# Optimization experiments

Measured on AMD Instinct MI355X. Metric: run time of the kernel, lower is better.

Reference implementation:

```python
import jax, jax.numpy as jnp
import numpy as np

E = 8        # n_experts
K = 2        # top_k
D = 1024     # n_embed
H = 2048     # moe_n_hidden
B, T = 4, 2048


def setup_inputs() -> dict:
    key = jax.random.key(0)
    ks = jax.random.split(key, 6)
    s = 0.02
    return {
        "x": jax.random.normal(ks[0], (B, T, D), dtype=jnp.float32),
        "Wr": jax.random.normal(ks[1], (D, E), dtype=jnp.float32) * s,   # router weight
        "W1": jax.random.normal(ks[2], (E, D, 2 * H), dtype=jnp.float32) * s,
        "b1": jnp.zeros((E, 2 * H), dtype=jnp.float32),
        "W2": jax.random.normal(ks[3], (E, H, D), dtype=jnp.float32) * s,
        "b2": jnp.zeros((E, D), dtype=jnp.float32),
    }


def reference(x, Wr, W1, b1, W2, b2):
    b, t, d = x.shape
    # router logits (noise=0, temp=1.0)
    z = jnp.einsum('btd,de->bte', x, Wr)                 # [B,T,E]
    vals, idx = jax.lax.top_k(z, K)                      # [B,T,K]
    gates = jax.nn.softmax(vals, axis=-1)                # [B,T,K]
    # combine weights per (token, expert): sum_k gate_k * 1[idx_k == e]
    onehot = jax.nn.one_hot(idx, E, dtype=x.dtype)       # [B,T,K,E]
    comb = jnp.einsum('btk,btke->bte', gates, onehot).reshape(b * t, E)
    xf = x.reshape(b * t, d)                             # [N,D]
    out = jnp.zeros_like(xf)
    for e in range(E):  # fixed small loop over structurally-distinct experts
        ab = xf @ W1[e] + b1[e]                          # [N,2H]
        a, bb = jnp.split(ab, 2, axis=-1)
        h = jax.nn.silu(a) * bb                          # swiGLU
        y = h @ W2[e] + b2[e]                            # [N,D]
        out = out + comb[:, e:e + 1] * y
    return out.reshape(b, t, d)
```

## Files before the change

### kernel.cpp

```cpp
#include <hip/hip_runtime.h>


#define N_TOK 8192
#define DIM   1024
#define HID   2048
#define NEXP  8
#define NK    (N_TOK * 2)
#define MAXT1 136
#define G1Y   272

typedef __attribute__((ext_vector_type(8))) short short8;
typedef __attribute__((ext_vector_type(4))) float f32x4;

#define BARX() __builtin_amdgcn_s_barrier()
#define FEN()  asm volatile("" ::: "memory")
#define VMW4() asm volatile("s_waitcnt vmcnt(4)" ::: "memory")
#define VMW0() asm volatile("s_waitcnt vmcnt(0)" ::: "memory")
#define PRIO(p) __builtin_amdgcn_s_setprio(p)

static __device__ __forceinline__ unsigned short f2bf(float f) {
  unsigned int u = __float_as_uint(f);
  u += 0x7fffu + ((u >> 16) & 1u);
  return (unsigned short)(u >> 16);
}

static __device__ __forceinline__ void glds16(const void* g, void* l) {
  __builtin_amdgcn_global_load_lds(
      (const __attribute__((address_space(1))) unsigned int*)g,
      (__attribute__((address_space(3))) unsigned int*)l, 16, 0, 0);
}

__device__ __forceinline__ void transpose_tile(const float* __restrict__ s,
                                               unsigned short* __restrict__ d,
                                               int R, int C, int c0, int r0,
                                               unsigned short (*tT)[68]) {
  int tid = threadIdx.x;
  int c = tid & 63, rq = tid >> 6;
#pragma unroll
  for (int q = 0; q < 4; ++q) {
    int rb = q * 16 + rq * 4;
    ushort4 v;
    v.x = f2bf(s[(size_t)(r0 + rb + 0) * C + c0 + c]);
    v.y = f2bf(s[(size_t)(r0 + rb + 1) * C + c0 + c]);
    v.z = f2bf(s[(size_t)(r0 + rb + 2) * C + c0 + c]);
    v.w = f2bf(s[(size_t)(r0 + rb + 3) * C + c0 + c]);
    *(ushort4*)&tT[c][rb] = v;
  }
  __syncthreads();
#pragma unroll
  for (int it = 0; it < 4; ++it) {
    int idx = it * 256 + tid;
    int cc = idx >> 4;
    int r4 = (idx & 15) * 4;
    *(ushort4*)(d + (size_t)(c0 + cc) * R + r0 + r4) = *(const ushort4*)&tT[cc][r4];
  }
}

__global__ __launch_bounds__(256) void prep_k(
    const float* __restrict__ x, const float* __restrict__ Wr,
    const float* __restrict__ W1,
    unsigned short* __restrict__ w1t,
    unsigned short* __restrict__ xb, int* __restrict__ te,
    float* __restrict__ tg) {
  __shared__ unsigned short tT[64][68];
  int bid = blockIdx.x;
  if (bid < 8192) {
    int z = bid >> 10, rem = bid & 1023;
    int c0 = (rem & 63) * 64, r0 = (rem >> 6) * 64;
    transpose_tile(W1 + (size_t)z * DIM * 2 * HID,
                   w1t + (size_t)z * DIM * 2 * HID, DIM, 2 * HID, c0, r0, tT);
  } else {
    int n = (bid - 8192) * 4 + (threadIdx.x >> 6);
    int lane = threadIdx.x & 63;
    float z[8];
#pragma unroll
    for (int e = 0; e < 8; ++e) z[e] = 0.f;
    const float* xr = x + (size_t)n * DIM;
    unsigned short* xbr = xb + (size_t)n * DIM;
#pragma unroll 4
    for (int i = 0; i < DIM / 64; ++i) {
      int d = lane + i * 64;
      float xv = xr[d];
      xbr[d] = f2bf(xv);
      float4 w0 = *(const float4*)(Wr + (size_t)d * 8);
      float4 w1 = *(const float4*)(Wr + (size_t)d * 8 + 4);
      z[0] += xv * w0.x; z[1] += xv * w0.y; z[2] += xv * w0.z; z[3] += xv * w0.w;
      z[4] += xv * w1.x; z[5] += xv * w1.y; z[6] += xv * w1.z; z[7] += xv * w1.w;
    }
    for (int off = 32; off; off >>= 1)
#pragma unroll
      for (int e = 0; e < 8; ++e) z[e] += __shfl_down(z[e], off);
    if (lane == 0) {
      int e0 = 0; float v0 = z[0];
#pragma unroll
      for (int e = 1; e < 8; ++e) if (z[e] > v0) { v0 = z[e]; e0 = e; }
      int e1 = -1; float v1 = -3.4e38f;
#pragma unroll
      for (int e = 0; e < 8; ++e) if (e != e0 && z[e] > v1) { v1 = z[e]; e1 = e; }
      float r = expf(v1 - v0);
      float s0 = 1.f / (1.f + r);
      te[n * 2] = e0; te[n * 2 + 1] = e1;
      tg[n * 2] = s0; tg[n * 2 + 1] = r * s0;
    }
  }
}

__global__ __launch_bounds__(1024) void sortscan_k(
    const int* __restrict__ te, const float* __restrict__ tg,
    int* __restrict__ offs, int* __restrict__ tl128,
    int* __restrict__ rows, float* __restrict__ rowg) {
  __shared__ int hist[8];
  __shared__ int curs[8];
  int tid = threadIdx.x;
  if (tid < 8) hist[tid] = 0;
  __syncthreads();
  for (int i = tid; i < NK; i += 1024) atomicAdd(&hist[te[i]], 1);
  __syncthreads();
  if (tid == 0) {
    int o = 0, t1 = 0;
    offs[0] = 0; tl128[0] = 0;
    for (int e = 0; e < NEXP; ++e) {
      curs[e] = o;
      o += hist[e];
      offs[e + 1] = o;
      t1 += (hist[e] + 127) >> 7;
      tl128[e + 1] = t1;
    }
  }
  __syncthreads();
  for (int i = tid; i < NK; i += 1024) {
    int e = te[i];
    int pos = atomicAdd(&curs[e], 1);
    rows[pos] = i >> 1;
    rowg[pos] = tg[i];
  }
}

template <int GID>
__global__ __launch_bounds__(256, 3) void moe_gemm3b(
    const unsigned short* __restrict__ Asrc,
    const unsigned short* __restrict__ Wt,
    const float* __restrict__ bias,
    unsigned short* __restrict__ hb,
    float* __restrict__ out,
    const int* __restrict__ rows,
    const float* __restrict__ rowg,
    const int* __restrict__ offs,
    const int* __restrict__ tl,
    const float* __restrict__ W2f,
    unsigned short* __restrict__ w2td,
    float* __restrict__ outz) {
  constexpr int KD = (GID == 0) ? DIM : HID;
  constexpr int NT = KD / 32;
  __shared__ unsigned short smem[24576];

  int bt = blockIdx.y;
  if (GID == 0 && bt >= MAXT1) {
    if (bt < MAXT1 + 128) {
      int t = (bt - MAXT1) * 32 + (int)blockIdx.x;
      int z = t >> 9, rem = t & 511;
      int c0 = (rem & 15) * 64, r0 = (rem >> 4) * 64;
      transpose_tile(W2f + (size_t)z * HID * DIM,
                     w2td + (size_t)z * HID * DIM, HID, DIM, c0, r0,
                     (unsigned short(*)[68])smem);
    } else {
      int t = (bt - MAXT1 - 128) * 32 + (int)blockIdx.x;
      float4* o4 = (float4*)outz;
      int idx = t * 256 + threadIdx.x;
#pragma unroll
      for (int i = 0; i < 32; ++i) o4[idx + i * 65536] = (float4){0.f, 0.f, 0.f, 0.f};
    }
    return;
  }
  if (bt >= tl[NEXP]) return;
  int e = 0;
  while (e < NEXP - 1 && bt >= tl[e + 1]) ++e;
  int rt = bt - tl[e];
  int base = offs[e];
  int cntE = offs[e + 1] - base;
  int row0 = rt * 128;
  int jb = blockIdx.x;

  int tid = threadIdx.x, lane = tid & 63, w = tid >> 6;
  int wr = w >> 1, wc = w & 1;

  int g8 = (((lane & 3) ^ ((lane >> 3) & 3)) * 8);
  const unsigned short* aP[2];
  const unsigned short* bP[2];
  int aD[2], bD[2];
#pragma unroll
  for (int s = 0; s < 2; ++s) {
    int rA = w * 16 + (lane >> 2) + s * 64;
    int rr = row0 + rA; rr = rr < cntE ? rr : cntE - 1;
    if (GID == 0) {
      int tok = rows[base + rr];
      aP[s] = Asrc + (size_t)tok * DIM + g8;
    } else {
      aP[s] = Asrc + (size_t)(base + rr) * HID + g8;
    }
    aD[s] = (w * 16 + s * 64) * 32;
    int rB = w * 16 + (lane >> 2) + s * 64;
    if (GID == 0) {
      int j0 = jb * 64;
      int u = rB & 63, wcb = rB >> 6;
      int hcol = j0 + wcb * 32 + (u & 31);
      int w1row = hcol + (u >> 5) * HID;
      bP[s] = Wt + ((size_t)e * 2 * HID + w1row) * DIM + g8;
    } else {
      bP[s] = Wt + ((size_t)e * DIM + (jb * 128 + rB)) * HID + g8;
    }
    bD[s] = (w * 16 + s * 64) * 32;
  }

  auto stg = [&](int t, int buf) {
    if (t < NT) {
      glds16(aP[0] + (size_t)t * 32, smem + buf * 4096 + aD[0]);
      glds16(aP[1] + (size_t)t * 32, smem + buf * 4096 + aD[1]);
      glds16(bP[0] + (size_t)t * 32, smem + 12288 + buf * 4096 + bD[0]);
      glds16(bP[1] + (size_t)t * 32, smem + 12288 + buf * 4096 + bD[1]);
    }
  };

  int kg = lane >> 4, coll = lane & 15;
  int koff = ((kg ^ ((lane >> 1) & 3)) * 8);
  unsigned aoff[4], boff[4];
#pragma unroll
  for (int m = 0; m < 4; ++m) aoff[m] = (unsigned)((wr * 64 + m * 16 + coll) * 32 + koff);
#pragma unroll
  for (int n = 0; n < 4; ++n) boff[n] = (unsigned)((wc * 64 + n * 16 + coll) * 32 + koff);

  f32x4 acc[4][4];
#pragma unroll
  for (int m = 0; m < 4; ++m)
#pragma unroll
    for (int n = 0; n < 4; ++n) acc[m][n] = (f32x4){0.f, 0.f, 0.f, 0.f};

  short8 a[4], b[4];

  stg(0, 0);
  stg(1, 1);

  int rb = 0;
  for (int t = 0; t < NT; ++t) {
    if (t == NT - 1) { VMW0(); } else { VMW4(); }
    FEN(); BARX(); FEN();
    int wb = rb + 2; if (wb >= 3) wb -= 3;
    stg(t + 2, wb);
#pragma unroll
    for (int m = 0; m < 4; ++m)
      a[m] = *(const short8*)(smem + rb * 4096 + aoff[m]);
#pragma unroll
    for (int n = 0; n < 4; ++n)
      b[n] = *(const short8*)(smem + 12288 + rb * 4096 + boff[n]);
    PRIO(1);
#pragma unroll
    for (int m = 0; m < 4; ++m)
#pragma unroll
      for (int n = 0; n < 4; ++n)
        acc[m][n] = __builtin_amdgcn_mfma_f32_16x16x32_bf16(a[m], b[n], acc[m][n], 0, 0, 0);
    PRIO(0);
    rb = (rb + 1 == 3) ? 0 : rb + 1;
  }

  int rowl = lane >> 4;
  if (GID == 0) {
    int j0 = jb * 64;
#pragma unroll
    for (int n = 0; n < 2; ++n) {
      int hcol = j0 + wc * 32 + n * 16 + coll;
      float ba = bias[e * 2 * HID + hcol];
      float bb = bias[e * 2 * HID + HID + hcol];
#pragma unroll
      for (int m = 0; m < 4; ++m)
#pragma unroll
        for (int j = 0; j < 4; ++j) {
          int grow = row0 + wr * 64 + m * 16 + rowl * 4 + j;
          if (grow < cntE) {
            float av = acc[m][n][j] + ba;
            float bv = acc[m][n + 2][j] + bb;
            float hv = av / (1.f + __expf(-av)) * bv;
            hb[(size_t)(base + grow) * HID + hcol] = f2bf(hv);
          }
        }
    }
  } else {
#pragma unroll
    for (int m = 0; m < 4; ++m)
#pragma unroll
      for (int j = 0; j < 4; ++j) {
        int grow = row0 + wr * 64 + m * 16 + rowl * 4 + j;
        if (grow < cntE) {
          int tok = rows[base + grow];
          float g = rowg[base + grow];
#pragma unroll
          for (int n = 0; n < 4; ++n) {
            int col = jb * 128 + wc * 64 + n * 16 + coll;
            atomicAdd(&out[(size_t)tok * DIM + col],
                      g * (acc[m][n][j] + bias[e * DIM + col]));
          }
        }
      }
  }
}

extern "C" void kernel_launch(void* const* d_in, const int* in_sizes, int n_in,
                              void* d_out, int out_size, void* d_ws, size_t ws_size,
                              hipStream_t stream) {
  (void)in_sizes; (void)n_in; (void)out_size;
  const float* x  = (const float*)d_in[0];
  const float* Wr = (const float*)d_in[1];
  const float* W1 = (const float*)d_in[2];
  const float* b1 = (const float*)d_in[3];
  const float* W2 = (const float*)d_in[4];
  const float* b2 = (const float*)d_in[5];
  float* out = (float*)d_out;
  char* ws = (char*)d_ws;

  const size_t o_xb   = 0;
  const size_t o_w1t  = o_xb   + (size_t)N_TOK * DIM * 2;
  const size_t o_w2t  = o_w1t  + (size_t)NEXP * 2 * HID * DIM * 2;
  const size_t o_hb   = o_w2t  + (size_t)NEXP * DIM * HID * 2;
  const size_t o_rows = o_hb   + (size_t)NK * HID * 2;
  const size_t o_rowg = o_rows + (size_t)NK * 4;
  const size_t o_te   = o_rowg + (size_t)NK * 4;
  const size_t o_tg   = o_te   + (size_t)NK * 4;
  const size_t o_offs = o_tg   + (size_t)NK * 4;
  const size_t o_t1   = o_offs + 64;
  const size_t need   = o_t1   + 64;
  if (ws_size < need) return;

  unsigned short* xb  = (unsigned short*)(ws + o_xb);
  unsigned short* w1t = (unsigned short*)(ws + o_w1t);
  unsigned short* w2t = (unsigned short*)(ws + o_w2t);
  unsigned short* hb  = (unsigned short*)(ws + o_hb);
  int*   rows = (int*)(ws + o_rows);
  float* rowg = (float*)(ws + o_rowg);
  int*   te   = (int*)(ws + o_te);
  float* tg   = (float*)(ws + o_tg);
  int*   offs = (int*)(ws + o_offs);
  int*   tl128 = (int*)(ws + o_t1);

  prep_k<<<10240, 256, 0, stream>>>(x, Wr, W1, w1t, xb, te, tg);
  sortscan_k<<<1, 1024, 0, stream>>>(te, tg, offs, tl128, rows, rowg);
  moe_gemm3b<0><<<dim3(HID / 64, G1Y), 256, 0, stream>>>(
      xb, w1t, b1, hb, nullptr, rows, rowg, offs, tl128, W2, w2t, out);
  moe_gemm3b<1><<<dim3(DIM / 128, MAXT1), 256, 0, stream>>>(
      hb, w2t, b2, nullptr, out, rows, rowg, offs, tl128, nullptr, nullptr, nullptr);
}
```

Measured before the change: 403.1 us.

## Split second expert GEMM into 8-wave ping-pong kernel with 128x256 tiles

```diff
diff --git a/kernel.cpp b/kernel.cpp
--- a/kernel.cpp
+++ b/kernel.cpp
@@ -15,6 +15,7 @@
 #define BARX() __builtin_amdgcn_s_barrier()
 #define FEN()  asm volatile("" ::: "memory")
 #define VMW4() asm volatile("s_waitcnt vmcnt(4)" ::: "memory")
+#define VMW2() asm volatile("s_waitcnt vmcnt(2)" ::: "memory")
 #define VMW0() asm volatile("s_waitcnt vmcnt(0)" ::: "memory")
 #define PRIO(p) __builtin_amdgcn_s_setprio(p)
 
@@ -136,26 +137,22 @@
   }
 }
 
-template <int GID>
-__global__ __launch_bounds__(256, 3) void moe_gemm3b(
+__global__ __launch_bounds__(256, 3) void gemm1_3b(
     const unsigned short* __restrict__ Asrc,
     const unsigned short* __restrict__ Wt,
     const float* __restrict__ bias,
     unsigned short* __restrict__ hb,
-    float* __restrict__ out,
     const int* __restrict__ rows,
-    const float* __restrict__ rowg,
     const int* __restrict__ offs,
     const int* __restrict__ tl,
     const float* __restrict__ W2f,
     unsigned short* __restrict__ w2td,
     float* __restrict__ outz) {
-  constexpr int KD = (GID == 0) ? DIM : HID;
-  constexpr int NT = KD / 32;
+  constexpr int NT = DIM / 32;
   __shared__ unsigned short smem[24576];
 
   int bt = blockIdx.y;
-  if (GID == 0 && bt >= MAXT1) {
+  if (bt >= MAXT1) {
     if (bt < MAXT1 + 128) {
       int t = (bt - MAXT1) * 32 + (int)blockIdx.x;
       int z = t >> 9, rem = t & 511;
@@ -192,23 +189,15 @@
   for (int s = 0; s < 2; ++s) {
     int rA = w * 16 + (lane >> 2) + s * 64;
     int rr = row0 + rA; rr = rr < cntE ? rr : cntE - 1;
-    if (GID == 0) {
-      int tok = rows[base + rr];
-      aP[s] = Asrc + (size_t)tok * DIM + g8;
-    } else {
-      aP[s] = Asrc + (size_t)(base + rr) * HID + g8;
-    }
+    int tok = rows[base + rr];
+    aP[s] = Asrc + (size_t)tok * DIM + g8;
     aD[s] = (w * 16 + s * 64) * 32;
     int rB = w * 16 + (lane >> 2) + s * 64;
-    if (GID == 0) {
-      int j0 = jb * 64;
-      int u = rB & 63, wcb = rB >> 6;
-      int hcol = j0 + wcb * 32 + (u & 31);
-      int w1row = hcol + (u >> 5) * HID;
-      bP[s] = Wt + ((size_t)e * 2 * HID + w1row) * DIM + g8;
-    } else {
-      bP[s] = Wt + ((size_t)e * DIM + (jb * 128 + rB)) * HID + g8;
-    }
+    int j0 = jb * 64;
+    int u = rB & 63, wcb = rB >> 6;
+    int hcol = j0 + wcb * 32 + (u & 31);
+    int w1row = hcol + (u >> 5) * HID;
+    bP[s] = Wt + ((size_t)e * 2 * HID + w1row) * DIM + g8;
     bD[s] = (w * 16 + s * 64) * 32;
   }
 
@@ -263,44 +252,188 @@
   }
 
   int rowl = lane >> 4;
-  if (GID == 0) {
-    int j0 = jb * 64;
-#pragma unroll
-    for (int n = 0; n < 2; ++n) {
-      int hcol = j0 + wc * 32 + n * 16 + coll;
-      float ba = bias[e * 2 * HID + hcol];
-      float bb = bias[e * 2 * HID + HID + hcol];
-#pragma unroll
-      for (int m = 0; m < 4; ++m)
-#pragma unroll
-        for (int j = 0; j < 4; ++j) {
-          int grow = row0 + wr * 64 + m * 16 + rowl * 4 + j;
-          if (grow < cntE) {
-            float av = acc[m][n][j] + ba;
-            float bv = acc[m][n + 2][j] + bb;
-            float hv = av / (1.f + __expf(-av)) * bv;
-            hb[(size_t)(base + grow) * HID + hcol] = f2bf(hv);
-          }
-        }
-    }
-  } else {
+  int j0 = jb * 64;
+#pragma unroll
+  for (int n = 0; n < 2; ++n) {
+    int hcol = j0 + wc * 32 + n * 16 + coll;
+    float ba = bias[e * 2 * HID + hcol];
+    float bb = bias[e * 2 * HID + HID + hcol];
 #pragma unroll
     for (int m = 0; m < 4; ++m)
 #pragma unroll
       for (int j = 0; j < 4; ++j) {
         int grow = row0 + wr * 64 + m * 16 + rowl * 4 + j;
         if (grow < cntE) {
-          int tok = rows[base + grow];
-          float g = rowg[base + grow];
-#pragma unroll
-          for (int n = 0; n < 4; ++n) {
-            int col = jb * 128 + wc * 64 + n * 16 + coll;
-            atomicAdd(&out[(size_t)tok * DIM + col],
-                      g * (acc[m][n][j] + bias[e * DIM + col]));
-          }
+          float av = acc[m][n][j] + ba;
+          float bv = acc[m][n + 2][j] + bb;
+          float hv = av / (1.f + __expf(-av)) * bv;
+          hb[(size_t)(base + grow) * HID + hcol] = f2bf(hv);
         }
       }
   }
+}
+
+__global__ __launch_bounds__(512, 2) void gemm2_8p(
+    const unsigned short* __restrict__ hb,
+    const unsigned short* __restrict__ w2t,
+    const float* __restrict__ bias,
+    float* __restrict__ out,
+    const int* __restrict__ rows,
+    const float* __restrict__ rowg,
+    const int* __restrict__ offs,
+    const int* __restrict__ tl) {
+  constexpr int NT = HID / 64;
+  constexpr int ASZ = 128 * 64;
+  __shared__ unsigned short smem[2 * ASZ + 2 * 16384];
+
+  int bt = blockIdx.y;
+  if (bt >= tl[NEXP]) return;
+  int e = 0;
+  while (e < NEXP - 1 && bt >= tl[e + 1]) ++e;
+  int rt = bt - tl[e];
+  int base = offs[e];
+  int cntE = offs[e + 1] - base;
+  int row0 = rt * 128;
+  int jb = blockIdx.x;
+
+  int tid = threadIdx.x, lane = tid & 63, w = tid >> 6;
+  int wr = w >> 2, wc = w & 3;
+
+  int g8 = (((lane & 7) ^ ((lane >> 3) & 7)) * 8);
+  const unsigned short* aP[2];
+  const unsigned short* bP[2][2];
+  int aD[2], bD[2][2];
+#pragma unroll
+  for (int hf = 0; hf < 2; ++hf) {
+    {
+      int q0 = w * 8;
+      int rbA = (q0 < 32 ? q0 : q0 + 32) + hf * 32;
+      int rA = rbA + (lane >> 3);
+      int rr = row0 + rA; rr = rr < cntE ? rr : cntE - 1;
+      aP[hf] = hb + (size_t)(base + rr) * HID + g8;
+      aD[hf] = rbA * 64;
+    }
+#pragma unroll
+    for (int s = 0; s < 2; ++s) {
+      int q0 = w * 16 + s * 8;
+      int rB = hf * 128 + q0 + (lane >> 3);
+      int j0 = jb * 256;
+      bP[hf][s] = w2t + ((size_t)e * DIM + (j0 + rB)) * HID + g8;
+      bD[hf][s] = (hf * 128 + q0) * 64;
+    }
+  }
+
+  auto stA = [&](int t, int hf) {
+    if (t < NT) glds16(aP[hf] + (size_t)t * 64, smem + (t & 1) * ASZ + aD[hf]);
+  };
+  auto stB = [&](int t, int hf) {
+    if (t < NT) {
+#pragma unroll
+      for (int s = 0; s < 2; ++s)
+        glds16(bP[hf][s] + (size_t)t * 64, smem + 2 * ASZ + (t & 1) * 16384 + bD[hf][s]);
+    }
+  };
+
+  int arow = wr * 64 + (lane & 15);
+  int brow = wc * 64 + (lane & 15);
+  int kg = lane >> 4, sx = lane & 7;
+  unsigned aoffs[2] = {(unsigned)(arow * 64 + ((kg ^ sx) * 8)),
+                       (unsigned)(arow * 64 + (((4 + kg) ^ sx) * 8))};
+  unsigned boffs[2] = {(unsigned)(brow * 64 + ((kg ^ sx) * 8)),
+                       (unsigned)(brow * 64 + (((4 + kg) ^ sx) * 8))};
+
+  f32x4 acc[4][4];
+#pragma unroll
+  for (int m = 0; m < 4; ++m)
+#pragma unroll
+    for (int n = 0; n < 4; ++n) acc[m][n] = (f32x4){0.f, 0.f, 0.f, 0.f};
+
+  short8 a[2][2], b[2][4];
+
+#define MFMA_Q(MB, NB)                                                        \
+  PRIO(1);                                                                    \
+  _Pragma("unroll") for (int ks = 0; ks < 2; ++ks)                            \
+  _Pragma("unroll") for (int m = 0; m < 2; ++m)                               \
+  _Pragma("unroll") for (int n = 0; n < 2; ++n)                               \
+    acc[(MB) + m][(NB) + n] = __builtin_amdgcn_mfma_f32_16x16x32_bf16(        \
+        a[ks][m], b[ks][(NB) + n], acc[(MB) + m][(NB) + n], 0, 0, 0);         \
+  PRIO(0)
+
+  stA(0, 0); stA(0, 1); stB(0, 0); stB(0, 1); stA(1, 0); stA(1, 1);
+  VMW2(); FEN(); BARX(); FEN();
+
+  for (int it = 0; it < NT / 2; ++it) {
+    int T = 2 * it;
+    bool notlast = (it < NT / 2 - 1);
+#pragma unroll
+    for (int half = 0; half < 2; ++half) {
+      unsigned Ab = half ? (unsigned)ASZ : 0u;
+      unsigned Bb = 2u * ASZ + (half ? 16384u : 0u);
+      int Tn = T + half;
+#pragma unroll
+      for (int ks = 0; ks < 2; ++ks) {
+#pragma unroll
+        for (int m = 0; m < 2; ++m)
+          a[ks][m] = *(const short8*)(smem + Ab + aoffs[ks] + m * 1024);
+#pragma unroll
+        for (int n = 0; n < 2; ++n)
+          b[ks][n] = *(const short8*)(smem + Bb + boffs[ks] + n * 1024);
+      }
+      stB(Tn + 1, 0);
+      FEN(); BARX(); FEN();
+      MFMA_Q(0, 0);
+      FEN(); BARX(); FEN();
+#pragma unroll
+      for (int ks = 0; ks < 2; ++ks)
+#pragma unroll
+        for (int n = 2; n < 4; ++n)
+          b[ks][n] = *(const short8*)(smem + Bb + boffs[ks] + n * 1024);
+      stB(Tn + 1, 1);
+      FEN(); BARX(); FEN();
+      MFMA_Q(0, 2);
+      FEN(); BARX(); FEN();
+#pragma unroll
+      for (int ks = 0; ks < 2; ++ks)
+#pragma unroll
+        for (int m = 0; m < 2; ++m)
+          a[ks][m] = *(const short8*)(smem + Ab + aoffs[ks] + (2 + m) * 1024);
+      stA(Tn + 2, 0);
+      FEN(); BARX(); FEN();
+      MFMA_Q(2, 2);
+      FEN(); BARX(); FEN();
+      stA(Tn + 2, 1);
+      FEN(); BARX(); FEN();
+      MFMA_Q(2, 0);
+      if (half == 0) {
+        if (notlast) { VMW2(); } else { VMW0(); }
+      } else {
+        VMW2();
+      }
+      FEN(); BARX(); FEN();
+    }
+  }
+#undef MFMA_Q
+
+  int rowl = lane >> 4, coll = lane & 15;
+  int j0 = jb * 256;
+  float bv[4];
+#pragma unroll
+  for (int n = 0; n < 4; ++n) bv[n] = bias[e * DIM + j0 + wc * 64 + n * 16 + coll];
+#pragma unroll
+  for (int m = 0; m < 4; ++m)
+#pragma unroll
+    for (int j = 0; j < 4; ++j) {
+      int grow = row0 + wr * 64 + m * 16 + rowl * 4 + j;
+      if (grow < cntE) {
+        int tok = rows[base + grow];
+        float g = rowg[base + grow];
+#pragma unroll
+        for (int n = 0; n < 4; ++n) {
+          int col = j0 + wc * 64 + n * 16 + coll;
+          atomicAdd(&out[(size_t)tok * DIM + col], g * (acc[m][n][j] + bv[n]));
+        }
+      }
+    }
 }
 
 extern "C" void kernel_launch(void* const* d_in, const int* in_sizes, int n_in,
@@ -342,8 +475,8 @@
 
   prep_k<<<10240, 256, 0, stream>>>(x, Wr, W1, w1t, xb, te, tg);
   sortscan_k<<<1, 1024, 0, stream>>>(te, tg, offs, tl128, rows, rowg);
-  moe_gemm3b<0><<<dim3(HID / 64, G1Y), 256, 0, stream>>>(
-      xb, w1t, b1, hb, nullptr, rows, rowg, offs, tl128, W2, w2t, out);
-  moe_gemm3b<1><<<dim3(DIM / 128, MAXT1), 256, 0, stream>>>(
-      hb, w2t, b2, nullptr, out, rows, rowg, offs, tl128, nullptr, nullptr, nullptr);
-}
+  gemm1_3b<<<dim3(HID / 64, G1Y), 256, 0, stream>>>(
+      xb, w1t, b1, hb, rows, offs, tl128, W2, w2t, out);
+  gemm2_8p<<<dim3(DIM / 256, MAXT1), 512, 0, stream>>>(
+      hb, w2t, b2, out, rows, rowg, offs, tl128);
+}
```

Result: faster. 393.6 us (-2.4%).
